# Performance work log

Measured on AMD Instinct MI355X. Metric: run time of the kernel, lower is better.

The kernel has to match this reference:

```python
import jax, jax.numpy as jnp
import numpy as np

N_NODES = 50000
N_EDGES = 800000
IN_CH = 128
OUT_CH = 64
HEADS = 2


def setup_inputs() -> dict:
    key = jax.random.key(0)
    k1, k2, k3, k4, k5 = jax.random.split(key, 5)
    x = jax.random.normal(k1, (N_NODES, IN_CH), dtype=jnp.float32)
    edge_index = jax.random.randint(k2, (2, N_EDGES), 0, N_NODES, dtype=jnp.int64)
    # nn.Linear(in, out*heads, bias=False): weight [out*heads, in]; store transposed [in, out*heads]
    W_lin = jax.random.normal(k3, (IN_CH, OUT_CH * HEADS), dtype=jnp.float32) * (1.0 / np.sqrt(IN_CH))
    att = jax.random.normal(k4, (1, HEADS, OUT_CH), dtype=jnp.float32) * 0.1
    W_out = jax.random.normal(k5, (OUT_CH * HEADS, OUT_CH), dtype=jnp.float32) * (1.0 / np.sqrt(OUT_CH * HEADS))
    b_out = jnp.zeros((OUT_CH,), dtype=jnp.float32)
    return {"x": x, "edge_index": edge_index, "W_lin": W_lin, "att": att,
            "W_out": W_out, "b_out": b_out}


def reference(x, edge_index, W_lin, att, W_out, b_out):
    N = x.shape[0]
    H = HEADS
    x_proj = x @ W_lin                      # [N, H*C]
    xp = x_proj.reshape(N, H, -1)           # [N, H, C]
    # edge_h = xp[row]*att + xp[col]*att; scores = edge_h.sum(-1).mean(heads)
    # -> per-node score s[n] = ((xp[n]*att).sum(-1)).mean(heads); edge score = s[row]+s[col]
    node_score = (xp * att).sum(-1).mean(axis=1)   # [N]
    row, col = edge_index[0], edge_index[1]
    scores = node_score[row] + node_score[col]     # [E]
    edge_weight = jax.nn.softmax(scores, axis=0)   # global softmax over all edges
    # sparse adj (row, col, w) @ x_proj_flat -> segment-sum over rows
    msg = edge_weight[:, None] * x_proj[col]       # [E, H*C]
    agg = jax.ops.segment_sum(msg, row, num_segments=N)  # [N, H*C]
    return jnp.tanh(agg @ W_out + b_out)           # [N, C]
```

## Files before the change

kernel.cpp:

```cpp
#include <hip/hip_runtime.h>
#include <hip/hip_fp16.h>
#include <math.h>

#define N_NODES 50000
#define N_EDGES 800000
#define NBUCK 196
#define BROWS 256
#define GRID_P 256
#define SLICE_CAP 48
#define EMAX 5120
#define EMAXP 6400
#define SENT 50000
#define SENTPAIR 0xC350C350u

typedef _Float16 h4 __attribute__((ext_vector_type(4)));
typedef float f32x4 __attribute__((ext_vector_type(4)));

__global__ __launch_bounds__(1024) void part_prep(
    const int* __restrict__ ei, const float* __restrict__ Wl,
    const float* __restrict__ att, const float* __restrict__ Wo,
    float* __restrict__ Wc, float* __restrict__ avec,
    float* __restrict__ Zp, unsigned* __restrict__ part,
    unsigned* __restrict__ cntm) {
  const int bid = blockIdx.x;
  const int tid = threadIdx.x;
  if (bid >= GRID_P) {
    const int pb = bid - GRID_P;
    if (pb < 8) {
      const int idx = pb * 1024 + tid;
      const int i = idx >> 6, j = idx & 63;
      float acc = 0.f;
      for (int m = 0; m < 128; ++m)
        acc = fmaf(Wl[i * 128 + m], Wo[m * 64 + j], acc);
      Wc[idx] = acc;
    } else {
      if (tid < 128) {
        float acc = 0.f;
        for (int m = 0; m < 128; ++m)
          acc = fmaf(Wl[tid * 128 + m], att[m], acc);
        avec[tid] = 0.5f * acc;
      } else if (tid == 128) {
        Zp[0] = 0.f;
      }
    }
    return;
  }
  __shared__ int cur[NBUCK];
  for (int i = tid; i < NBUCK; i += 1024) cur[i] = 0;
  __syncthreads();
  const int G = GRID_P * 1024;
  for (int e = bid * 1024 + tid; e < N_EDGES; e += 2 * G) {
    const int e1 = e + G;
    const bool v1 = e1 < N_EDGES;
    const int r0 = ei[e];
    const int c0 = ei[N_EDGES + e];
    int r1 = 0, c1 = 0;
    if (v1) {
      r1 = ei[e1];
      c1 = ei[N_EDGES + e1];
    }
    const int p0 = atomicAdd(&cur[r0 >> 8], 1);
    if (p0 < SLICE_CAP)
      part[((size_t)(r0 >> 8) * GRID_P + bid) * SLICE_CAP + p0] =
          ((unsigned)(r0 & 255) << 16) | (unsigned)c0;
    if (v1) {
      const int p1 = atomicAdd(&cur[r1 >> 8], 1);
      if (p1 < SLICE_CAP)
        part[((size_t)(r1 >> 8) * GRID_P + bid) * SLICE_CAP + p1] =
            ((unsigned)(r1 & 255) << 16) | (unsigned)c1;
    }
  }
  __syncthreads();
  for (int i = tid; i < NBUCK; i += 1024)
    cntm[i * GRID_P + bid] = (unsigned)min(cur[i], SLICE_CAP);
}

__global__ __launch_bounds__(256) void proj_score(
    const float* __restrict__ x, const float* __restrict__ Wc,
    const float* __restrict__ avec, __half2* __restrict__ yh,
    float* __restrict__ a) {
  __shared__ __half xs[64 * 132];
  __shared__ __half Wcs[64 * 132];
  const int tid = threadIdx.x;
  const int row0 = blockIdx.x * 64;

  if (blockIdx.x == 0) {
    if (tid < 32) yh[(size_t)SENT * 32 + tid] = __floats2half2_rn(0.f, 0.f);
    else if (tid == 32) a[SENT] = 0.f;
  }

  for (int m = 0; m < 8; ++m) {
    const int i = m * 256 + tid;
    const int row = i >> 5, c4 = i & 31;
    const int r = row0 + row;
    float4 v = make_float4(0.f, 0.f, 0.f, 0.f);
    if (r < N_NODES) v = ((const float4*)x)[(size_t)r * 32 + c4];
    float p = v.x * avec[c4 * 4] + v.y * avec[c4 * 4 + 1] +
              v.z * avec[c4 * 4 + 2] + v.w * avec[c4 * 4 + 3];
#pragma unroll
    for (int off = 1; off < 32; off <<= 1) p += __shfl_xor(p, off);
    if ((tid & 31) == 0 && r < N_NODES) a[r] = __expf(p);
    *(__half2*)&xs[row * 132 + c4 * 4]     = __floats2half2_rn(v.x, v.y);
    *(__half2*)&xs[row * 132 + c4 * 4 + 2] = __floats2half2_rn(v.z, v.w);
  }
  for (int i = tid; i < 2048; i += 256) {
    const int k = i >> 4, c4 = i & 15;
    const float4 w = ((const float4*)Wc)[i];
    Wcs[(c4 * 4 + 0) * 132 + k] = __float2half(w.x);
    Wcs[(c4 * 4 + 1) * 132 + k] = __float2half(w.y);
    Wcs[(c4 * 4 + 2) * 132 + k] = __float2half(w.z);
    Wcs[(c4 * 4 + 3) * 132 + k] = __float2half(w.w);
  }
  __syncthreads();

  const int w = tid >> 6;
  const int l = tid & 63;
  const int lr = l & 15;
  const int lg = l >> 4;

  f32x4 acc[4];
#pragma unroll
  for (int ct = 0; ct < 4; ++ct) acc[ct] = (f32x4){0.f, 0.f, 0.f, 0.f};

#pragma unroll
  for (int ks = 0; ks < 8; ++ks) {
    const h4 xb = *(const h4*)&xs[(w * 16 + lr) * 132 + ks * 16 + lg * 4];
#pragma unroll
    for (int ct = 0; ct < 4; ++ct) {
      const h4 wa = *(const h4*)&Wcs[(ct * 16 + lr) * 132 + ks * 16 + lg * 4];
      acc[ct] = __builtin_amdgcn_mfma_f32_16x16x16f16(wa, xb, acc[ct], 0, 0, 0);
    }
  }

  const int r = row0 + w * 16 + lr;
  if (r < N_NODES) {
    struct __align__(8) H4 { __half2 a, b; };
#pragma unroll
    for (int ct = 0; ct < 4; ++ct) {
      H4 st;
      st.a = __floats2half2_rn(acc[ct][0], acc[ct][1]);
      st.b = __floats2half2_rn(acc[ct][2], acc[ct][3]);
      *(H4*)&yh[(size_t)r * 32 + ct * 8 + lg * 2] = st;
    }
  }
}

__global__ __launch_bounds__(1024) void build_csr(
    const unsigned* __restrict__ part, const unsigned* __restrict__ cntm,
    const float* __restrict__ a, float* __restrict__ Zp,
    unsigned short* __restrict__ nbr_g, int* __restrict__ rp_g) {
  __shared__ unsigned eb[EMAX];
  __shared__ unsigned short nbr_s[EMAXP];
  __shared__ int scnt[GRID_P], soff[GRID_P];
  __shared__ int hist[BROWS], rp[BROWS + 1], cur2[BROWS];
  __shared__ int wsum[4];
  __shared__ float red[16];
  const int k = blockIdx.x;
  const int tid = threadIdx.x;
  const int lane = tid & 63;
  const int wv = tid >> 6;

  if (tid < 800)
    ((uint4*)nbr_s)[tid] = make_uint4(SENTPAIR, SENTPAIR, SENTPAIR, SENTPAIR);

  int myc = 0;
  if (tid < GRID_P) {
    myc = (int)cntm[(size_t)k * GRID_P + tid];
    scnt[tid] = myc;
  }
  if (tid < BROWS) hist[tid] = 0;
  int incl = 0;
  if (tid < GRID_P) {
    incl = myc;
#pragma unroll
    for (int off = 1; off < 64; off <<= 1) {
      const int n = __shfl_up(incl, off);
      if (lane >= off) incl += n;
    }
    if (lane == 63) wsum[wv] = incl;
  }
  __syncthreads();
  if (tid < GRID_P) {
    int woff = 0;
    for (int i = 0; i < wv; ++i) woff += wsum[i];
    soff[tid] = woff + incl - myc;
  }
  int total = wsum[0] + wsum[1] + wsum[2] + wsum[3];
  if (total > EMAX) total = EMAX;
  __syncthreads();
#pragma unroll 4
  for (int b2 = wv; b2 < GRID_P; b2 += 16) {
    const int c = scnt[b2];
    const int dst = soff[b2] + lane;
    if (lane < c && dst < EMAX)
      eb[dst] = part[((size_t)k * GRID_P + b2) * SLICE_CAP + lane];
  }
  __syncthreads();

  float z = 0.f;
  const int rbase = k * BROWS;
  for (int i = tid; i < total; i += 1024) {
    const unsigned u = eb[i];
    atomicAdd(&hist[u >> 16], 1);
    z = fmaf(a[rbase + (int)(u >> 16)], a[u & 0xFFFFu], z);
  }
#pragma unroll
  for (int off = 32; off >= 1; off >>= 1) z += __shfl_xor(z, off);
  if ((tid & 63) == 0) red[tid >> 6] = z;
  __syncthreads();
  if (tid == 0) {
    float t = 0.f;
#pragma unroll
    for (int i = 0; i < 16; ++i) t += red[i];
    atomicAdd(Zp, t);
  }

  int hincl = 0, pv = 0;
  if (tid < BROWS) {
    const int hv = hist[tid];
    pv = (hv + 7) & ~7;
    hincl = pv;
#pragma unroll
    for (int off = 1; off < 64; off <<= 1) {
      const int n = __shfl_up(hincl, off);
      if (lane >= off) hincl += n;
    }
    if (lane == 63) wsum[wv] = hincl;
  }
  __syncthreads();
  if (tid < BROWS) {
    int woff = 0;
    for (int i = 0; i < wv; ++i) woff += wsum[i];
    const int excl = woff + hincl - pv;
    rp[tid] = excl;
    cur2[tid] = excl;
    if (tid == BROWS - 1) rp[BROWS] = excl + pv;
  }
  __syncthreads();
  for (int i = tid; i < total; i += 1024) {
    const unsigned u = eb[i];
    const int pos = atomicAdd(&cur2[u >> 16], 1);
    nbr_s[pos] = (unsigned short)(u & 0xFFFFu);
  }
  __syncthreads();

  const int ptot = rp[BROWS];
  uint4* dst = (uint4*)&nbr_g[(size_t)k * EMAXP];
  const uint4* srcv = (const uint4*)nbr_s;
  for (int i = tid; i < (ptot >> 3); i += 1024) dst[i] = srcv[i];
  for (int i = tid; i <= BROWS; i += 1024) rp_g[k * (BROWS + 1) + i] = rp[i];
}

__global__ __launch_bounds__(256) void gather(
    const unsigned short* __restrict__ nbr_g, const int* __restrict__ rp_g,
    const __half2* __restrict__ yh, const float* __restrict__ a,
    const float* __restrict__ Zp, const float* __restrict__ bias,
    float* __restrict__ out) {
  const int k = blockIdx.x >> 4;
  const int seg = blockIdx.x & 15;
  const int tid = threadIdx.x;
  const int g = tid >> 5;
  const int cp = tid & 31;
  const float invZ = 1.f / Zp[0];
  const unsigned short* nb = &nbr_g[(size_t)k * EMAXP];
  const int* rpk = &rp_g[k * (BROWS + 1)];
#pragma unroll
  for (int ri = 0; ri < 2; ++ri) {
    const int rlo = seg * 16 + g * 2 + ri;
    const int r = k * BROWS + rlo;
    if (r >= N_NODES) continue;
    const int beg = rpk[rlo];
    const int d = rpk[rlo + 1] - beg;
    float2 acc = make_float2(0.f, 0.f);
    for (int i = 0; i < d; i += 8) {
      const uint4 nv = *(const uint4*)&nb[beg + i];
      int c[8];
      c[0] = nv.x & 0xFFFF; c[1] = nv.x >> 16;
      c[2] = nv.y & 0xFFFF; c[3] = nv.y >> 16;
      c[4] = nv.z & 0xFFFF; c[5] = nv.z >> 16;
      c[6] = nv.w & 0xFFFF; c[7] = nv.w >> 16;
      float av[8];
      float2 v[8];
#pragma unroll
      for (int j = 0; j < 8; ++j) av[j] = a[c[j]];
#pragma unroll
      for (int j = 0; j < 8; ++j)
        v[j] = __half22float2(yh[(size_t)c[j] * 32 + cp]);
#pragma unroll
      for (int j = 0; j < 8; ++j) {
        acc.x = fmaf(av[j], v[j].x, acc.x);
        acc.y = fmaf(av[j], v[j].y, acc.y);
      }
    }
    const float scale = a[r] * invZ;
    float2 o;
    o.x = tanhf(fmaf(acc.x, scale, bias[cp * 2]));
    o.y = tanhf(fmaf(acc.y, scale, bias[cp * 2 + 1]));
    *(float2*)&out[(size_t)r * 64 + cp * 2] = o;
  }
}

extern "C" void kernel_launch(void* const* d_in, const int* in_sizes, int n_in,
                              void* d_out, int out_size, void* d_ws,
                              size_t ws_size, hipStream_t stream) {
  const float* x   = (const float*)d_in[0];
  const int*   ei  = (const int*)d_in[1];
  const float* Wl  = (const float*)d_in[2];
  const float* att = (const float*)d_in[3];
  const float* Wo  = (const float*)d_in[4];
  const float* b   = (const float*)d_in[5];
  float* out = (float*)d_out;

  float* ws = (float*)d_ws;
  float*          a     = ws;
  __half2*        yh    = (__half2*)(ws + 50176);
  float*          Zp    = ws + 1650208;
  float*          Wc    = ws + 1650212;
  float*          avec  = ws + 1658404;
  unsigned*       part  = (unsigned*)(ws + 1658532);
  unsigned*       cntm  = (unsigned*)(ws + 4066980);
  unsigned short* nbr_g = (unsigned short*)(ws + 4117156);
  int*            rp_g  = (int*)(ws + 4744356);

  part_prep<<<GRID_P + 9, 1024, 0, stream>>>(ei, Wl, att, Wo, Wc, avec, Zp,
                                             part, cntm);
  proj_score<<<(N_NODES + 63) / 64, 256, 0, stream>>>(x, Wc, avec, yh, a);
  build_csr<<<NBUCK, 1024, 0, stream>>>(part, cntm, a, Zp, nbr_g, rp_g);
  gather<<<NBUCK * 16, 256, 0, stream>>>(nbr_g, rp_g, yh, a, Zp, b, out);
}
```

Baseline: 63.92 us.

## Fuse edge partitioning and node projection into one kernel launch

Merges the edge-partition kernel and the projection/score kernel into a single launch. Extra blocks each recompute the combined weight matrix and attention vector into shared memory, then run the MFMA projection with x read straight from global memory. Partition blocks now stage their bucket slices in shared memory and write them out as contiguous per-bucket runs instead of scattered stores. This removes one launch and the global Wc/avec round trip, at the cost of each of the 196 projection blocks redoing the 128x128x64 weight product.

```diff
diff --git a/kernel.cpp b/kernel.cpp
--- a/kernel.cpp
+++ b/kernel.cpp
@@ -16,124 +16,133 @@
 typedef _Float16 h4 __attribute__((ext_vector_type(4)));
 typedef float f32x4 __attribute__((ext_vector_type(4)));
 
-__global__ __launch_bounds__(1024) void part_prep(
-    const int* __restrict__ ei, const float* __restrict__ Wl,
-    const float* __restrict__ att, const float* __restrict__ Wo,
-    float* __restrict__ Wc, float* __restrict__ avec,
-    float* __restrict__ Zp, unsigned* __restrict__ part,
-    unsigned* __restrict__ cntm) {
+union ShD1 {
+  struct {
+    int cur[NBUCK];
+    unsigned sl[NBUCK * SLICE_CAP];
+  } q;
+  struct {
+    __half Wcs[64 * 132];
+    float avs[128];
+  } p;
+};
+
+__global__ __launch_bounds__(1024, 8) void part_proj(
+    const int* __restrict__ ei, const float* __restrict__ x,
+    const float* __restrict__ Wl, const float* __restrict__ att,
+    const float* __restrict__ Wo, float* __restrict__ Zp,
+    float* __restrict__ a, __half2* __restrict__ yh,
+    unsigned* __restrict__ part, unsigned* __restrict__ cntm) {
+  __shared__ ShD1 sh;
   const int bid = blockIdx.x;
   const int tid = threadIdx.x;
-  if (bid >= GRID_P) {
-    const int pb = bid - GRID_P;
-    if (pb < 8) {
-      const int idx = pb * 1024 + tid;
-      const int i = idx >> 6, j = idx & 63;
-      float acc = 0.f;
-      for (int m = 0; m < 128; ++m)
-        acc = fmaf(Wl[i * 128 + m], Wo[m * 64 + j], acc);
-      Wc[idx] = acc;
-    } else {
-      if (tid < 128) {
-        float acc = 0.f;
-        for (int m = 0; m < 128; ++m)
-          acc = fmaf(Wl[tid * 128 + m], att[m], acc);
-        avec[tid] = 0.5f * acc;
-      } else if (tid == 128) {
-        Zp[0] = 0.f;
+
+  if (bid < GRID_P) {
+    for (int i = tid; i < NBUCK; i += 1024) sh.q.cur[i] = 0;
+    __syncthreads();
+    const int G = GRID_P * 1024;
+    for (int e = bid * 1024 + tid; e < N_EDGES; e += 2 * G) {
+      const int e1 = e + G;
+      const bool v1 = e1 < N_EDGES;
+      const int r0 = ei[e];
+      const int c0 = ei[N_EDGES + e];
+      int r1 = 0, c1 = 0;
+      if (v1) {
+        r1 = ei[e1];
+        c1 = ei[N_EDGES + e1];
       }
-    }
+      const int b0 = r0 >> 8;
+      const int p0 = atomicAdd(&sh.q.cur[b0], 1);
+      if (p0 < SLICE_CAP)
+        sh.q.sl[b0 * SLICE_CAP + p0] =
+            ((unsigned)(r0 & 255) << 16) | (unsigned)c0;
+      if (v1) {
+        const int b1 = r1 >> 8;
+        const int p1 = atomicAdd(&sh.q.cur[b1], 1);
+        if (p1 < SLICE_CAP)
+          sh.q.sl[b1 * SLICE_CAP + p1] =
+              ((unsigned)(r1 & 255) << 16) | (unsigned)c1;
+      }
+    }
+    __syncthreads();
+    const int lane = tid & 63;
+    const int wv = tid >> 6;
+    for (int b2 = wv; b2 < NBUCK; b2 += 16) {
+      const int n = min(sh.q.cur[b2], SLICE_CAP);
+      if (lane < n)
+        part[((size_t)b2 * GRID_P + bid) * SLICE_CAP + lane] =
+            sh.q.sl[b2 * SLICE_CAP + lane];
+    }
+    for (int i = tid; i < NBUCK; i += 1024)
+      cntm[i * GRID_P + bid] = (unsigned)min(sh.q.cur[i], SLICE_CAP);
     return;
   }
-  __shared__ int cur[NBUCK];
-  for (int i = tid; i < NBUCK; i += 1024) cur[i] = 0;
-  __syncthreads();
-  const int G = GRID_P * 1024;
-  for (int e = bid * 1024 + tid; e < N_EDGES; e += 2 * G) {
-    const int e1 = e + G;
-    const bool v1 = e1 < N_EDGES;
-    const int r0 = ei[e];
-    const int c0 = ei[N_EDGES + e];
-    int r1 = 0, c1 = 0;
-    if (v1) {
-      r1 = ei[e1];
-      c1 = ei[N_EDGES + e1];
-    }
-    const int p0 = atomicAdd(&cur[r0 >> 8], 1);
-    if (p0 < SLICE_CAP)
-      part[((size_t)(r0 >> 8) * GRID_P + bid) * SLICE_CAP + p0] =
-          ((unsigned)(r0 & 255) << 16) | (unsigned)c0;
-    if (v1) {
-      const int p1 = atomicAdd(&cur[r1 >> 8], 1);
-      if (p1 < SLICE_CAP)
-        part[((size_t)(r1 >> 8) * GRID_P + bid) * SLICE_CAP + p1] =
-            ((unsigned)(r1 & 255) << 16) | (unsigned)c1;
-    }
-  }
-  __syncthreads();
-  for (int i = tid; i < NBUCK; i += 1024)
-    cntm[i * GRID_P + bid] = (unsigned)min(cur[i], SLICE_CAP);
-}
-
-__global__ __launch_bounds__(256) void proj_score(
-    const float* __restrict__ x, const float* __restrict__ Wc,
-    const float* __restrict__ avec, __half2* __restrict__ yh,
-    float* __restrict__ a) {
-  __shared__ __half xs[64 * 132];
-  __shared__ __half Wcs[64 * 132];
-  const int tid = threadIdx.x;
-  const int row0 = blockIdx.x * 64;
-
-  if (blockIdx.x == 0) {
-    if (tid < 32) yh[(size_t)SENT * 32 + tid] = __floats2half2_rn(0.f, 0.f);
-    else if (tid == 32) a[SENT] = 0.f;
-  }
-
-  for (int m = 0; m < 8; ++m) {
-    const int i = m * 256 + tid;
-    const int row = i >> 5, c4 = i & 31;
-    const int r = row0 + row;
-    float4 v = make_float4(0.f, 0.f, 0.f, 0.f);
-    if (r < N_NODES) v = ((const float4*)x)[(size_t)r * 32 + c4];
-    float p = v.x * avec[c4 * 4] + v.y * avec[c4 * 4 + 1] +
-              v.z * avec[c4 * 4 + 2] + v.w * avec[c4 * 4 + 3];
-#pragma unroll
-    for (int off = 1; off < 32; off <<= 1) p += __shfl_xor(p, off);
-    if ((tid & 31) == 0 && r < N_NODES) a[r] = __expf(p);
-    *(__half2*)&xs[row * 132 + c4 * 4]     = __floats2half2_rn(v.x, v.y);
-    *(__half2*)&xs[row * 132 + c4 * 4 + 2] = __floats2half2_rn(v.z, v.w);
-  }
-  for (int i = tid; i < 2048; i += 256) {
-    const int k = i >> 4, c4 = i & 15;
-    const float4 w = ((const float4*)Wc)[i];
-    Wcs[(c4 * 4 + 0) * 132 + k] = __float2half(w.x);
-    Wcs[(c4 * 4 + 1) * 132 + k] = __float2half(w.y);
-    Wcs[(c4 * 4 + 2) * 132 + k] = __float2half(w.z);
-    Wcs[(c4 * 4 + 3) * 132 + k] = __float2half(w.w);
-  }
-  __syncthreads();
-
-  const int w = tid >> 6;
+
+  const int pb = bid - GRID_P;
+  if (tid < 128) {
+    float acc = 0.f;
+    for (int m = 0; m < 128; ++m)
+      acc = fmaf(Wl[tid * 128 + m], att[m], acc);
+    sh.p.avs[tid] = 0.5f * acc;
+  }
+  for (int e8 = 0; e8 < 8; ++e8) {
+    const int idx = e8 * 1024 + tid;
+    const int i = idx >> 6, j = idx & 63;
+    float acc = 0.f;
+    for (int m = 0; m < 128; ++m)
+      acc = fmaf(Wl[i * 128 + m], Wo[m * 64 + j], acc);
+    sh.p.Wcs[j * 132 + i] = __float2half(acc);
+  }
+  if (pb == 0) {
+    if (tid == 1023) a[SENT] = 0.f;
+    if (tid == 959) Zp[0] = 0.f;
+    if (tid >= 960 && tid < 992)
+      yh[(size_t)SENT * 32 + (tid - 960)] = __floats2half2_rn(0.f, 0.f);
+  }
+  __syncthreads();
+
+  const int g4 = tid >> 8;
+  const int t = pb * 4 + g4;
+  const int row0 = t * 64;
+  if (row0 >= N_NODES) return;
+  const int w = (tid >> 6) & 3;
   const int l = tid & 63;
   const int lr = l & 15;
   const int lg = l >> 4;
+  const int r = row0 + w * 16 + lr;
+  const bool valid = r < N_NODES;
+  const float* xrow = x + (size_t)(valid ? r : 0) * 128;
 
   f32x4 acc[4];
 #pragma unroll
   for (int ct = 0; ct < 4; ++ct) acc[ct] = (f32x4){0.f, 0.f, 0.f, 0.f};
+  float pdot = 0.f;
 
 #pragma unroll
   for (int ks = 0; ks < 8; ++ks) {
-    const h4 xb = *(const h4*)&xs[(w * 16 + lr) * 132 + ks * 16 + lg * 4];
+    float4 xv = *(const float4*)(xrow + ks * 16 + lg * 4);
+    if (!valid) xv = make_float4(0.f, 0.f, 0.f, 0.f);
+    pdot += xv.x * sh.p.avs[ks * 16 + lg * 4] +
+            xv.y * sh.p.avs[ks * 16 + lg * 4 + 1] +
+            xv.z * sh.p.avs[ks * 16 + lg * 4 + 2] +
+            xv.w * sh.p.avs[ks * 16 + lg * 4 + 3];
+    h4 xb;
+    xb[0] = (_Float16)xv.x;
+    xb[1] = (_Float16)xv.y;
+    xb[2] = (_Float16)xv.z;
+    xb[3] = (_Float16)xv.w;
 #pragma unroll
     for (int ct = 0; ct < 4; ++ct) {
-      const h4 wa = *(const h4*)&Wcs[(ct * 16 + lr) * 132 + ks * 16 + lg * 4];
+      const h4 wa =
+          *(const h4*)&sh.p.Wcs[(ct * 16 + lr) * 132 + ks * 16 + lg * 4];
       acc[ct] = __builtin_amdgcn_mfma_f32_16x16x16f16(wa, xb, acc[ct], 0, 0, 0);
     }
   }
-
-  const int r = row0 + w * 16 + lr;
-  if (r < N_NODES) {
+  pdot += __shfl_xor(pdot, 16);
+  pdot += __shfl_xor(pdot, 32);
+  if (lg == 0 && valid) a[r] = __expf(pdot);
+
+  if (valid) {
     struct __align__(8) H4 { __half2 a, b; };
 #pragma unroll
     for (int ct = 0; ct < 4; ++ct) {
@@ -145,7 +154,7 @@
   }
 }
 
-__global__ __launch_bounds__(1024) void build_csr(
+__global__ __launch_bounds__(1024) void build_z(
     const unsigned* __restrict__ part, const unsigned* __restrict__ cntm,
     const float* __restrict__ a, float* __restrict__ Zp,
     unsigned short* __restrict__ nbr_g, int* __restrict__ rp_g) {
@@ -162,7 +171,6 @@
 
   if (tid < 800)
     ((uint4*)nbr_s)[tid] = make_uint4(SENTPAIR, SENTPAIR, SENTPAIR, SENTPAIR);
-
   int myc = 0;
   if (tid < GRID_P) {
     myc = (int)cntm[(size_t)k * GRID_P + tid];
@@ -196,7 +204,6 @@
       eb[dst] = part[((size_t)k * GRID_P + b2) * SLICE_CAP + lane];
   }
   __syncthreads();
-
   float z = 0.f;
   const int rbase = k * BROWS;
   for (int i = tid; i < total; i += 1024) {
@@ -214,7 +221,6 @@
     for (int i = 0; i < 16; ++i) t += red[i];
     atomicAdd(Zp, t);
   }
-
   int hincl = 0, pv = 0;
   if (tid < BROWS) {
     const int hv = hist[tid];
@@ -243,7 +249,6 @@
     nbr_s[pos] = (unsigned short)(u & 0xFFFFu);
   }
   __syncthreads();
-
   const int ptot = rp[BROWS];
   uint4* dst = (uint4*)&nbr_g[(size_t)k * EMAXP];
   const uint4* srcv = (const uint4*)nbr_s;
@@ -315,16 +320,13 @@
   float*          a     = ws;
   __half2*        yh    = (__half2*)(ws + 50176);
   float*          Zp    = ws + 1650208;
-  float*          Wc    = ws + 1650212;
-  float*          avec  = ws + 1658404;
   unsigned*       part  = (unsigned*)(ws + 1658532);
   unsigned*       cntm  = (unsigned*)(ws + 4066980);
   unsigned short* nbr_g = (unsigned short*)(ws + 4117156);
   int*            rp_g  = (int*)(ws + 4744356);
 
-  part_prep<<<GRID_P + 9, 1024, 0, stream>>>(ei, Wl, att, Wo, Wc, avec, Zp,
-                                             part, cntm);
-  proj_score<<<(N_NODES + 63) / 64, 256, 0, stream>>>(x, Wc, avec, yh, a);
-  build_csr<<<NBUCK, 1024, 0, stream>>>(part, cntm, a, Zp, nbr_g, rp_g);
+  part_proj<<<GRID_P + 196, 1024, 0, stream>>>(ei, x, Wl, att, Wo, Zp, a, yh,
+                                               part, cntm);
+  build_z<<<NBUCK, 1024, 0, stream>>>(part, cntm, a, Zp, nbr_g, rp_g);
   gather<<<NBUCK * 16, 256, 0, stream>>>(nbr_g, rp_g, yh, a, Zp, b, out);
 }
```

New measurement: 107.2 us. 1.68x slower.
